# Kernel tuning notes

Measured on AMD Instinct MI355X. Metric: run time of the kernel, lower is better.

The kernel has to match this reference:

```python
import jax, jax.numpy as jnp
import numpy as np

N, B, C, K, H = 65536, 4, 512, 256, 8


def setup_inputs() -> dict:
    key = jax.random.key(0)
    ks = jax.random.split(key, 6)
    feat = jax.random.normal(ks[0], (N, C), dtype=jnp.float32)
    cls_tokens = jax.random.normal(ks[1], (B, C), dtype=jnp.float32)
    Wqkv = jax.random.normal(ks[2], (C, 3 * C), dtype=jnp.float32) * 0.02
    bqkv = jnp.zeros((3 * C,), dtype=jnp.float32)
    Wproj = jax.random.normal(ks[3], (C, C), dtype=jnp.float32) * 0.02
    bproj = jnp.zeros((C,), dtype=jnp.float32)
    order = jax.random.permutation(ks[4], N)          # serialized order (permutation)
    inverse = jnp.argsort(order)                       # its inverse
    offset = jnp.arange(1, B + 1) * (N // B)           # equal-size point clouds, divisible by K
    return {"feat": feat, "cls_tokens": cls_tokens, "Wqkv": Wqkv, "bqkv": bqkv,
            "Wproj": Wproj, "bproj": bproj, "order": order, "inverse": inverse,
            "offset": offset, "patch_size": K, "num_heads": H}


def reference(feat, cls_tokens, Wqkv, bqkv, Wproj, bproj, order, inverse, offset, patch_size, num_heads):
    n, c = feat.shape
    b = offset.shape[0]
    k = patch_size
    h = num_heads
    dh = c // h
    scale = dh ** -0.5
    n_chunks = n // k

    # qkv projection, gather into serialized order
    qkv = (feat @ Wqkv + bqkv)[order]                  # [N, 3C]
    cls_qkv = cls_tokens @ Wqkv + bqkv                 # [B, 3C]

    # chunk -> batch assignment (offsets are chunk-aligned here)
    chunk_starts = jnp.arange(n_chunks) * k
    batch_id = jnp.searchsorted(offset, chunk_starts, side="right")  # [n_chunks]
    acc = jax.nn.one_hot(batch_id, b, dtype=feat.dtype)              # [n_chunks, B]
    agg = acc.T / acc.T.sum(axis=1, keepdims=True)                   # [B, n_chunks]

    cls_per_chunk = acc @ cls_qkv                                    # [n_chunks, 3C]
    qkv_c = qkv.reshape(n_chunks, k, 3 * c)
    qkv_c = jnp.concatenate([cls_per_chunk[:, None, :], qkv_c], axis=1)  # [n_chunks, K+1, 3C]

    qkv_c = qkv_c.reshape(n_chunks, k + 1, 3, h, dh)
    q = qkv_c[:, :, 0].transpose(0, 2, 1, 3)           # [n_chunks, H, K+1, dh]
    kk = qkv_c[:, :, 1].transpose(0, 2, 1, 3)
    v = qkv_c[:, :, 2].transpose(0, 2, 1, 3)

    # upcast_attention / upcast_softmax = True
    attn = jnp.einsum("nhqd,nhkd->nhqk", q.astype(jnp.float32) * scale, kk.astype(jnp.float32))
    attn = jax.nn.softmax(attn, axis=-1).astype(feat.dtype)
    out = jnp.einsum("nhqk,nhkd->nhqd", attn, v)       # [n_chunks, H, K+1, dh]
    out = out.transpose(0, 2, 1, 3).reshape(n_chunks, k + 1, c)

    feat_out = out[:, 1:, :].reshape(-1, c)[inverse]   # scatter back to original order
    feat_out = feat_out @ Wproj + bproj                # proj (proj_drop is identity in eval)
    cls_feat = agg @ out[:, 0, :]                      # [B, C] (no proj, per source)
    return feat_out, cls_feat
```

## Files before the change

### kernel.cpp

```cpp
#include <hip/hip_runtime.h>


typedef float  floatx4 __attribute__((ext_vector_type(4)));
typedef __bf16 bf16x8  __attribute__((ext_vector_type(8)));

__device__ __forceinline__ __bf16 f2bf(float x) {
  unsigned u = __builtin_bit_cast(unsigned, x);
  u = u + 0x7FFFu + ((u >> 16) & 1u);
  unsigned short h = (unsigned short)(u >> 16);
  return __builtin_bit_cast(__bf16, h);
}

__device__ __forceinline__ floatx4 mfma_16x16x32(bf16x8 a, bf16x8 b, floatx4 c) {
  return __builtin_amdgcn_mfma_f32_16x16x32_bf16(a, b, c, 0, 0, 0);
}

__device__ __forceinline__ void gload16(const void* g, void* l) {
  __builtin_amdgcn_global_load_lds(
      (const __attribute__((address_space(1))) unsigned int*)g,
      (__attribute__((address_space(3))) unsigned int*)l, 16, 0, 0);
}

__global__ void cast_gather_feat(const float* __restrict__ feat,
                                 const int* __restrict__ order,
                                 __bf16* __restrict__ dst) {
  long i = ((long)blockIdx.x * blockDim.x + threadIdx.x) * 8;
  int row = (int)(i >> 9);
  int col = (int)(i & 511);
  const float* sp = feat + (long)order[row] * 512 + col;
  float4 a = *(const float4*)sp;
  float4 b = *(const float4*)(sp + 4);
  bf16x8 o;
  o[0] = f2bf(a.x); o[1] = f2bf(a.y); o[2] = f2bf(a.z); o[3] = f2bf(a.w);
  o[4] = f2bf(b.x); o[5] = f2bf(b.y); o[6] = f2bf(b.z); o[7] = f2bf(b.w);
  *(bf16x8*)(dst + i) = o;
}

__global__ void transpose_cast(const float* __restrict__ W, __bf16* __restrict__ Wt,
                               int K, int N) {
  __shared__ float tile[32][33];
  const int n0 = blockIdx.x * 32, k0 = blockIdx.y * 32;
  const int c = threadIdx.x & 31, r8 = threadIdx.x >> 5;
#pragma unroll
  for (int i = 0; i < 4; ++i) {
    int r = r8 + i * 8;
    tile[r][c] = W[(long)(k0 + r) * N + n0 + c];
  }
  __syncthreads();
#pragma unroll
  for (int i = 0; i < 4; ++i) {
    int r = r8 + i * 8;
    Wt[(long)(n0 + r) * K + k0 + c] = f2bf(tile[c][r]);
  }
}

__global__ void cls_qkv_kernel(const float* __restrict__ cls_tokens,
                               const float* __restrict__ Wqkv,
                               const float* __restrict__ bqkv,
                               __bf16* __restrict__ clsqkv, int N3) {
  __shared__ float red[256];
  const int c = threadIdx.x & 63, part = threadIdx.x >> 6;
  const int o = blockIdx.x * 64 + c;
  const int b = o / N3, n = o - b * N3;
  float sv = 0.f;
  const int kst = part * 128;
  for (int k = kst; k < kst + 128; ++k)
    sv += cls_tokens[b * 512 + k] * Wqkv[(long)k * N3 + n];
  red[threadIdx.x] = sv;
  __syncthreads();
  if (part == 0)
    clsqkv[o] = f2bf(red[c] + red[c + 64] + red[c + 128] + red[c + 192] + bqkv[n]);
}

template <int OUT_F32>
__global__ __launch_bounds__(256, 2) void gemm_bt(
    const __bf16* __restrict__ A, const __bf16* __restrict__ Bt,
    const float* __restrict__ bias, void* __restrict__ C,
    int N, int K) {
  __shared__ __align__(16) __bf16 As[128 * 64];
  __shared__ __align__(16) __bf16 Bs[128 * 64];
  const int tid = threadIdx.x;
  const int wave = tid >> 6, lane = tid & 63;
  const int quad = lane >> 4, l15 = lane & 15;
  const int wr = wave >> 1, wc = wave & 1;
  const long m0 = (long)blockIdx.y * 128;
  const int n0 = blockIdx.x * 128;
  const int srow8 = lane >> 3;
  const int sc8p = lane & 7;

  floatx4 zero = {0.f, 0.f, 0.f, 0.f};
  floatx4 acc[4][4];
#pragma unroll
  for (int i = 0; i < 4; ++i)
#pragma unroll
    for (int j = 0; j < 4; ++j) acc[i][j] = zero;

  for (int kt = 0; kt < K; kt += 64) {
    __syncthreads();
#pragma unroll
    for (int i = 0; i < 4; ++i) {
      const int rbase = i * 32 + wave * 8;
      const int row = rbase + srow8;
      const int c8 = sc8p ^ (row & 7);
      gload16(A + (m0 + row) * K + kt + c8 * 8, As + rbase * 64);
      gload16(Bt + (long)(n0 + row) * K + kt + c8 * 8, Bs + rbase * 64);
    }
    __syncthreads();
#pragma unroll
    for (int ks = 0; ks < 2; ++ks) {
      bf16x8 af[4], bfr[4];
#pragma unroll
      for (int mi = 0; mi < 4; ++mi) {
        int row = wr * 64 + mi * 16 + l15;
        int c8 = ks * 4 + quad;
        af[mi] = *(const bf16x8*)(As + row * 64 + ((c8 ^ (row & 7)) << 3));
      }
#pragma unroll
      for (int ni = 0; ni < 4; ++ni) {
        int row = wc * 64 + ni * 16 + l15;
        int c8 = ks * 4 + quad;
        bfr[ni] = *(const bf16x8*)(Bs + row * 64 + ((c8 ^ (row & 7)) << 3));
      }
#pragma unroll
      for (int mi = 0; mi < 4; ++mi)
#pragma unroll
        for (int ni = 0; ni < 4; ++ni)
          acc[mi][ni] = mfma_16x16x32(af[mi], bfr[ni], acc[mi][ni]);
    }
  }
#pragma unroll
  for (int mi = 0; mi < 4; ++mi) {
#pragma unroll
    for (int ni = 0; ni < 4; ++ni) {
      const int col = n0 + wc * 64 + ni * 16 + l15;
      const float bb = bias[col];
#pragma unroll
      for (int r = 0; r < 4; ++r) {
        const long row = m0 + wr * 64 + mi * 16 + quad * 4 + r;
        float v = acc[mi][ni][r] + bb;
        if (OUT_F32)
          ((float*)C)[row * N + col] = v;
        else
          ((__bf16*)C)[row * N + col] = f2bf(v);
      }
    }
  }
}

__global__ __launch_bounds__(256, 2) void attn_kernel(
    const __bf16* __restrict__ qkv,
    const __bf16* __restrict__ clsqkv,
    const int* __restrict__ order,
    const int* __restrict__ offset,
    __bf16* __restrict__ outO,
    float* __restrict__ outcls,
    int B) {
  __shared__ __align__(16) __bf16 Ks[272 * 64];
  __shared__ __align__(16) __bf16 Vt[64 * 264 + 64];
  __shared__ __align__(16) __bf16 Pbuf[4 * 16 * 40];
  const int chunk = blockIdx.x & 255;
  const int h = blockIdx.x >> 8;
  const int tid = threadIdx.x;
  const int wave = tid >> 6, lane = tid & 63;
  const int quad = lane >> 4, l15 = lane & 15;
  const int cs = chunk << 8;
  int batch = 0;
  for (int b = 0; b < B; ++b) batch += (offset[b] <= cs) ? 1 : 0;
  const unsigned clsoff =
      (unsigned)((const char*)(clsqkv + (long)batch * 1536) - (const char*)qkv);

  const int qoffB = h * 128;
  const int koffB = 1024 + h * 128;
  const int voffB = 2048 + h * 128;

  auto rowoff = [&](int t) -> unsigned {
    int tt = (t <= 256) ? t : 256;
    return (tt == 0) ? clsoff : (unsigned)(cs + tt - 1) * 3072u;
  };

  {
    const int rsub = lane >> 3, c8 = lane & 7;
    for (int i = wave; i < 34; i += 4) {
      int r = i * 8 + rsub;
      gload16((const char*)qkv + rowoff(r) + koffB + ((c8 ^ (r & 7)) << 4),
              Ks + i * 512);
    }
  }

  {
    const int rsub = lane >> 3, c8 = lane & 7;
#pragma unroll
    for (int p = 0; p < 8; ++p) {
      int t = p * 32 + wave * 8 + rsub;
      unsigned ro = (t == 0) ? clsoff : (unsigned)(cs + t - 1) * 3072u;
      bf16x8 v = *(const bf16x8*)((const char*)qkv + ro + voffB + c8 * 16);
#pragma unroll
      for (int j = 0; j < 8; ++j)
        Vt[(c8 * 8 + j) * 264 + c8 * 8 + t] = v[j];
    }
    if (tid < 8) {
      bf16x8 v = *(const bf16x8*)((const char*)qkv +
                                  (unsigned)(cs + 255) * 3072u + voffB + tid * 16);
#pragma unroll
      for (int j = 0; j < 8; ++j)
        Vt[(tid * 8 + j) * 264 + tid * 8 + 256] = v[j];
    }
  }
  __syncthreads();

  int vbase[4];
#pragma unroll
  for (int ni = 0; ni < 4; ++ni) {
    int d = ni * 16 + l15;
    vbase[ni] = d * 264 + ((ni * 2 + (l15 >> 3)) & 7) * 8;
  }
  float v256[4];
#pragma unroll
  for (int ni = 0; ni < 4; ++ni) v256[ni] = (float)Vt[vbase[ni] + 256];
  __bf16* Pw = Pbuf + wave * (16 * 40);
  const int sw = l15 & 7;
  const __bf16* kb = Ks + l15 * 64;

  for (int rt = wave; rt < 17; rt += 4) {
    const unsigned qo = rowoff(rt * 16 + l15);
    bf16x8 qf0 = *(const bf16x8*)((const char*)qkv + qo + qoffB + quad * 16);
    bf16x8 qf1 = *(const bf16x8*)((const char*)qkv + qo + qoffB + 64 + quad * 16);

    floatx4 zero = {0.f, 0.f, 0.f, 0.f};
    floatx4 s[17];
#pragma unroll
    for (int i = 0; i < 17; ++i) s[i] = zero;
#pragma unroll
    for (int k2 = 0; k2 < 17; ++k2) {
      const __bf16* kr = kb + k2 * 1024;
      bf16x8 kf0 = *(const bf16x8*)(kr + ((quad ^ sw) << 3));
      bf16x8 kf1 = *(const bf16x8*)(kr + (((quad + 4) ^ sw) << 3));
      s[k2] = mfma_16x16x32(qf0, kf0, s[k2]);
      s[k2] = mfma_16x16x32(qf1, kf1, s[k2]);
    }

    float mx[4] = {-3.0e38f, -3.0e38f, -3.0e38f, -3.0e38f};
#pragma unroll
    for (int k2 = 0; k2 < 16; ++k2)
#pragma unroll
      for (int r = 0; r < 4; ++r) mx[r] = fmaxf(mx[r], s[k2][r]);
#pragma unroll
    for (int r = 0; r < 4; ++r) {
      float v = (l15 == 0) ? s[16][r] : -3.0e38f;
      s[16][r] = v;
      mx[r] = fmaxf(mx[r], v);
    }
#pragma unroll
    for (int off = 1; off < 16; off <<= 1)
#pragma unroll
      for (int r = 0; r < 4; ++r) mx[r] = fmaxf(mx[r], __shfl_xor(mx[r], off, 16));
    const float c1 = 0.125f * 1.44269504f;
    float mb[4], sum[4] = {0.f, 0.f, 0.f, 0.f};
#pragma unroll
    for (int r = 0; r < 4; ++r) mb[r] = mx[r] * c1;
#pragma unroll
    for (int k2 = 0; k2 < 17; ++k2)
#pragma unroll
      for (int r = 0; r < 4; ++r) {
        float e = __builtin_amdgcn_exp2f(fmaf(s[k2][r], c1, -mb[r]));
        s[k2][r] = e;
        sum[r] += e;
      }
#pragma unroll
    for (int off = 1; off < 16; off <<= 1)
#pragma unroll
      for (int r = 0; r < 4; ++r) sum[r] += __shfl_xor(sum[r], off, 16);
    float rl[4];
#pragma unroll
    for (int r = 0; r < 4; ++r) rl[r] = 1.0f / sum[r];

    floatx4 o[4];
#pragma unroll
    for (int i = 0; i < 4; ++i) o[i] = zero;
#pragma unroll
    for (int ks = 0; ks < 8; ++ks) {
#pragma unroll
      for (int half = 0; half < 2; ++half) {
        int kt2 = ks * 2 + half;
#pragma unroll
        for (int r = 0; r < 4; ++r)
          Pw[(quad * 4 + r) * 40 + half * 16 + l15] = f2bf(s[kt2][r]);
      }
      asm volatile("s_waitcnt lgkmcnt(0)" ::: "memory");
      bf16x8 pf = *(const bf16x8*)(Pw + l15 * 40 + quad * 8);
#pragma unroll
      for (int ni = 0; ni < 4; ++ni) {
        bf16x8 vf = *(const bf16x8*)(Vt + vbase[ni] + ks * 32 + quad * 8);
        o[ni] = mfma_16x16x32(pf, vf, o[ni]);
      }
    }
    float p256[4];
#pragma unroll
    for (int r = 0; r < 4; ++r) p256[r] = __shfl(s[16][r], lane & 48, 64);
#pragma unroll
    for (int ni = 0; ni < 4; ++ni)
#pragma unroll
      for (int r = 0; r < 4; ++r)
        o[ni][r] = (o[ni][r] + p256[r] * v256[ni]) * rl[r];

#pragma unroll
    for (int r = 0; r < 4; ++r) {
      int q = rt * 16 + quad * 4 + r;
      if (q > 256) continue;
      if (q == 0) {
#pragma unroll
        for (int ni = 0; ni < 4; ++ni)
          outcls[(long)chunk * 512 + h * 64 + ni * 16 + l15] = o[ni][r];
      } else {
        long orow = (long)order[cs + q - 1];
#pragma unroll
        for (int ni = 0; ni < 4; ++ni)
          outO[orow * 512 + h * 64 + ni * 16 + l15] = f2bf(o[ni][r]);
      }
    }
  }
}

__global__ void cls_feat_kernel(const float* __restrict__ outcls,
                                const int* __restrict__ offset,
                                float* __restrict__ dst, int B, int C) {
  int i = blockIdx.x * blockDim.x + threadIdx.x;
  if (i >= B * C) return;
  int b = i / C, c = i - b * C;
  int st = (b == 0) ? 0 : offset[b - 1];
  int en = offset[b];
  int c0 = st >> 8, c1 = en >> 8;
  float s = 0.f;
  for (int ch = c0; ch < c1; ++ch) s += outcls[(long)ch * C + c];
  dst[i] = s / (float)(c1 - c0);
}

extern "C" void kernel_launch(void* const* d_in, const int* in_sizes, int n_in,
                              void* d_out, int out_size, void* d_ws, size_t ws_size,
                              hipStream_t stream) {
  const float* feat       = (const float*)d_in[0];
  const float* cls_tokens = (const float*)d_in[1];
  const float* Wqkv       = (const float*)d_in[2];
  const float* bqkv       = (const float*)d_in[3];
  const float* Wproj      = (const float*)d_in[4];
  const float* bproj      = (const float*)d_in[5];
  const int*   order      = (const int*)d_in[6];
  const int*   offset     = (const int*)d_in[8];
  const int B = in_sizes[8];

  char* ws = (char*)d_ws;
  __bf16* qkv    = (__bf16*)(ws);
  __bf16* featb  = (__bf16*)(ws + 201326592);
  __bf16* outO   = featb;
  __bf16* wqkvT  = (__bf16*)(ws + 268435456);
  __bf16* wprojT = (__bf16*)(ws + 270008320);
  __bf16* clsqkv = (__bf16*)(ws + 270532608);
  float*  outcls = (float*)(ws + 270544896);

  float* feat_out = (float*)d_out;
  float* cls_out  = feat_out + (long)65536 * 512;

  cast_gather_feat<<<16384, 256, 0, stream>>>(feat, order, featb);
  transpose_cast<<<dim3(48, 16), 256, 0, stream>>>(Wqkv, wqkvT, 512, 1536);
  transpose_cast<<<dim3(16, 16), 256, 0, stream>>>(Wproj, wprojT, 512, 512);
  cls_qkv_kernel<<<96, 256, 0, stream>>>(cls_tokens, Wqkv, bqkv, clsqkv, 1536);

  gemm_bt<0><<<dim3(12, 512), 256, 0, stream>>>(featb, wqkvT, bqkv, (void*)qkv, 1536, 512);

  attn_kernel<<<2048, 256, 0, stream>>>(qkv, clsqkv, order, offset, outO, outcls, B);

  gemm_bt<1><<<dim3(4, 512), 256, 0, stream>>>(outO, wprojT, bproj, (void*)feat_out, 512, 512);

  cls_feat_kernel<<<8, 256, 0, stream>>>(outcls, offset, cls_out, B, 512);
}
```

Baseline: 611.1 us.

## Fuse feature gather and bf16 cast into QKV GEMM A-tile loads

Removes the separate cast_gather_feat pass: the QKV GEMM now loads fp32 feature rows through the order permutation, converts them to bf16 in registers and writes them into swizzled LDS, prefetching the next K-tile into registers. This avoids writing and re-reading a 64 MB bf16 gathered copy. Both GEMMs also switch to a 1D grid with an XCD-aware block remap so neighbouring tiles land on the same chiplet for L2 reuse. In exchange, the fused kernel reads fp32 A data once per column block (12 times), which adds register pressure and uncoalesced gathered loads.

```diff
diff --git a/kernel.cpp b/kernel.cpp
--- a/kernel.cpp
+++ b/kernel.cpp
@@ -19,21 +19,6 @@
   __builtin_amdgcn_global_load_lds(
       (const __attribute__((address_space(1))) unsigned int*)g,
       (__attribute__((address_space(3))) unsigned int*)l, 16, 0, 0);
-}
-
-__global__ void cast_gather_feat(const float* __restrict__ feat,
-                                 const int* __restrict__ order,
-                                 __bf16* __restrict__ dst) {
-  long i = ((long)blockIdx.x * blockDim.x + threadIdx.x) * 8;
-  int row = (int)(i >> 9);
-  int col = (int)(i & 511);
-  const float* sp = feat + (long)order[row] * 512 + col;
-  float4 a = *(const float4*)sp;
-  float4 b = *(const float4*)(sp + 4);
-  bf16x8 o;
-  o[0] = f2bf(a.x); o[1] = f2bf(a.y); o[2] = f2bf(a.z); o[3] = f2bf(a.w);
-  o[4] = f2bf(b.x); o[5] = f2bf(b.y); o[6] = f2bf(b.z); o[7] = f2bf(b.w);
-  *(bf16x8*)(dst + i) = o;
 }
 
 __global__ void transpose_cast(const float* __restrict__ W, __bf16* __restrict__ Wt,
@@ -72,7 +57,110 @@
     clsqkv[o] = f2bf(red[c] + red[c + 64] + red[c + 128] + red[c + 192] + bqkv[n]);
 }
 
-template <int OUT_F32>
+__global__ __launch_bounds__(256, 2) void gemm_qkv_fused(
+    const float* __restrict__ feat,
+    const int* __restrict__ order,
+    const __bf16* __restrict__ Bt,
+    const float* __restrict__ bias,
+    __bf16* __restrict__ C,
+    int N, int K) {
+  __shared__ __align__(16) __bf16 As[128 * 64];
+  __shared__ __align__(16) __bf16 Bs[128 * 64];
+  __shared__ int ords[128];
+  const int tid = threadIdx.x;
+  const int wave = tid >> 6, lane = tid & 63;
+  const int quad = lane >> 4, l15 = lane & 15;
+  const int wr = wave >> 1, wc = wave & 1;
+  const int per = gridDim.x >> 3;
+  const int work = (blockIdx.x & 7) * per + (blockIdx.x >> 3);
+  const int rowblk = work / 12, colblk = work - rowblk * 12;
+  const long m0 = (long)rowblk * 128;
+  const int n0 = colblk * 128;
+  const int srow8 = lane >> 3;
+  const int sc8p = lane & 7;
+
+  if (tid < 128) ords[tid] = order[m0 + tid];
+  __syncthreads();
+
+  const int arow = tid >> 1;
+  const int ahalf = tid & 1;
+  const long abase = (long)ords[arow] * 512;
+
+  floatx4 zero = {0.f, 0.f, 0.f, 0.f};
+  floatx4 acc[4][4];
+#pragma unroll
+  for (int i = 0; i < 4; ++i)
+#pragma unroll
+    for (int j = 0; j < 4; ++j) acc[i][j] = zero;
+
+  float4 areg[8];
+#pragma unroll
+  for (int j = 0; j < 8; ++j)
+    areg[j] = *(const float4*)(feat + abase + ahalf * 32 + j * 4);
+
+  for (int kt = 0; kt < K; kt += 64) {
+    __syncthreads();
+#pragma unroll
+    for (int i = 0; i < 4; ++i) {
+      const int rbase = i * 32 + wave * 8;
+      const int row = rbase + srow8;
+      const int c8 = sc8p ^ (row & 7);
+      gload16(Bt + (long)(n0 + row) * K + kt + c8 * 8, Bs + rbase * 64);
+    }
+#pragma unroll
+    for (int jj = 0; jj < 4; ++jj) {
+      float4 lo = areg[2 * jj], hi = areg[2 * jj + 1];
+      bf16x8 o;
+      o[0] = (__bf16)lo.x; o[1] = (__bf16)lo.y; o[2] = (__bf16)lo.z; o[3] = (__bf16)lo.w;
+      o[4] = (__bf16)hi.x; o[5] = (__bf16)hi.y; o[6] = (__bf16)hi.z; o[7] = (__bf16)hi.w;
+      const int c8 = ahalf * 4 + jj;
+      *(bf16x8*)(As + arow * 64 + ((c8 ^ (arow & 7)) << 3)) = o;
+    }
+    if (kt + 64 < K) {
+      const long nb = abase + kt + 64;
+#pragma unroll
+      for (int j = 0; j < 8; ++j)
+        areg[j] = *(const float4*)(feat + nb + ahalf * 32 + j * 4);
+    }
+    __syncthreads();
+#pragma unroll
+    for (int ks = 0; ks < 2; ++ks) {
+      bf16x8 af[4], bfr[4];
+#pragma unroll
+      for (int mi = 0; mi < 4; ++mi) {
+        int row = wr * 64 + mi * 16 + l15;
+        int c8 = ks * 4 + quad;
+        af[mi] = *(const bf16x8*)(As + row * 64 + ((c8 ^ (row & 7)) << 3));
+      }
+#pragma unroll
+      for (int ni = 0; ni < 4; ++ni) {
+        int row = wc * 64 + ni * 16 + l15;
+        int c8 = ks * 4 + quad;
+        bfr[ni] = *(const bf16x8*)(Bs + row * 64 + ((c8 ^ (row & 7)) << 3));
+      }
+#pragma unroll
+      for (int mi = 0; mi < 4; ++mi)
+#pragma unroll
+        for (int ni = 0; ni < 4; ++ni)
+          acc[mi][ni] = mfma_16x16x32(af[mi], bfr[ni], acc[mi][ni]);
+    }
+  }
+#pragma unroll
+  for (int mi = 0; mi < 4; ++mi) {
+#pragma unroll
+    for (int ni = 0; ni < 4; ++ni) {
+      const int col = n0 + wc * 64 + ni * 16 + l15;
+      const float bb = bias[col];
+#pragma unroll
+      for (int r = 0; r < 4; ++r) {
+        const long row = m0 + wr * 64 + mi * 16 + quad * 4 + r;
+        C[row * N + col] = f2bf(acc[mi][ni][r] + bb);
+      }
+    }
+  }
+}
+
+template <int OUT_F32, int COLS>
 __global__ __launch_bounds__(256, 2) void gemm_bt(
     const __bf16* __restrict__ A, const __bf16* __restrict__ Bt,
     const float* __restrict__ bias, void* __restrict__ C,
@@ -83,8 +171,11 @@
   const int wave = tid >> 6, lane = tid & 63;
   const int quad = lane >> 4, l15 = lane & 15;
   const int wr = wave >> 1, wc = wave & 1;
-  const long m0 = (long)blockIdx.y * 128;
-  const int n0 = blockIdx.x * 128;
+  const int per = gridDim.x >> 3;
+  const int work = (blockIdx.x & 7) * per + (blockIdx.x >> 3);
+  const int rowblk = work / COLS, colblk = work - rowblk * COLS;
+  const long m0 = (long)rowblk * 128;
+  const int n0 = colblk * 128;
   const int srow8 = lane >> 3;
   const int sc8p = lane & 7;
 
@@ -350,8 +441,7 @@
 
   char* ws = (char*)d_ws;
   __bf16* qkv    = (__bf16*)(ws);
-  __bf16* featb  = (__bf16*)(ws + 201326592);
-  __bf16* outO   = featb;
+  __bf16* outO   = (__bf16*)(ws + 201326592);
   __bf16* wqkvT  = (__bf16*)(ws + 268435456);
   __bf16* wprojT = (__bf16*)(ws + 270008320);
   __bf16* clsqkv = (__bf16*)(ws + 270532608);
@@ -360,16 +450,15 @@
   float* feat_out = (float*)d_out;
   float* cls_out  = feat_out + (long)65536 * 512;
 
-  cast_gather_feat<<<16384, 256, 0, stream>>>(feat, order, featb);
   transpose_cast<<<dim3(48, 16), 256, 0, stream>>>(Wqkv, wqkvT, 512, 1536);
   transpose_cast<<<dim3(16, 16), 256, 0, stream>>>(Wproj, wprojT, 512, 512);
   cls_qkv_kernel<<<96, 256, 0, stream>>>(cls_tokens, Wqkv, bqkv, clsqkv, 1536);
 
-  gemm_bt<0><<<dim3(12, 512), 256, 0, stream>>>(featb, wqkvT, bqkv, (void*)qkv, 1536, 512);
+  gemm_qkv_fused<<<6144, 256, 0, stream>>>(feat, order, wqkvT, bqkv, qkv, 1536, 512);
 
   attn_kernel<<<2048, 256, 0, stream>>>(qkv, clsqkv, order, offset, outO, outcls, B);
 
-  gemm_bt<1><<<dim3(4, 512), 256, 0, stream>>>(outO, wprojT, bproj, (void*)feat_out, 512, 512);
+  gemm_bt<1, 4><<<2048, 256, 0, stream>>>(outO, wprojT, bproj, (void*)feat_out, 512, 512);
 
   cls_feat_kernel<<<8, 256, 0, stream>>>(outcls, offset, cls_out, B, 512);
 }
```

After: 688.5 us. +12.7%, slower.
